# Kernel tuning notes

Measured on AMD Instinct MI355X. Metric: run time of the kernel, lower is better.

## Reference

```python
import jax, jax.numpy as jnp
import numpy as np

jax.config.update("jax_enable_x64", True)  # original computes distances in float64

B, NL, NP, C, H, G, A, E = 16, 64, 512, 128, 256, 10, 14, 2048
BN_EPS = 1e-5


def _static_indices():
    # ragged graph sizes (batch_num_nodes) -> static scatter / valid-pair indices
    counts_l = np.array([32 if i % 2 == 0 else 64 for i in range(B)])
    counts_p = np.array([256 if i % 2 == 0 else 512 for i in range(B)])
    idx_l = np.concatenate([b * NL + np.arange(c) for b, c in enumerate(counts_l)])
    idx_p = np.concatenate([b * NP + np.arange(c) for b, c in enumerate(counts_p)])
    mask_l = np.zeros(B * NL, bool); mask_l[idx_l] = True
    mask_p = np.zeros(B * NP, bool); mask_p[idx_p] = True
    mask = mask_l.reshape(B, NL, 1) & mask_p.reshape(B, 1, NP)  # C_mask
    pair_flat = np.nonzero(mask.reshape(-1))[0]                 # row-major == torch C[C_mask] order
    pb = pair_flat // (NL * NP)
    rem = pair_flat % (NL * NP)
    pair_l = pb * NL + rem // NP
    pair_p = pb * NP + rem % NP
    return idx_l, idx_p, pair_flat, pair_l, pair_p, pb, len(idx_l), len(idx_p)


def setup_inputs() -> dict:
    idx_l, idx_p, pair_flat, pair_l, pair_p, pair_b, TL, TP = _static_indices()
    ks = jax.random.split(jax.random.key(0), 14)
    f32 = jnp.float32
    s = 0.02
    return {
        "h_l": jax.random.normal(ks[0], (TL, C), f32),
        "h_p": jax.random.normal(ks[1], (TP, C), f32),
        "lig_pos": jax.random.normal(ks[2], (TL, 3), f32) * 5.0,
        "prot_pos": jax.random.normal(ks[3], (TP, A, 3), f32) * 5.0,
        "edge_src": jax.random.randint(ks[4], (E,), 0, TL),
        "edge_dst": jax.random.randint(ks[5], (E,), 0, TL),
        "idx_l": jnp.asarray(idx_l), "idx_p": jnp.asarray(idx_p),
        "pair_flat": jnp.asarray(pair_flat), "pair_l": jnp.asarray(pair_l),
        "pair_p": jnp.asarray(pair_p), "pair_b": jnp.asarray(pair_b),
        "W1": jax.random.normal(ks[6], (2 * C, H), f32) * s, "b1": jnp.zeros(H, f32),
        "gamma": jnp.ones(H, f32), "beta": jnp.zeros(H, f32),
        "rmean": jnp.zeros(H, f32), "rvar": jnp.ones(H, f32),
        "Wpi": jax.random.normal(ks[7], (H, G * A), f32) * s, "bpi": jnp.zeros(G * A, f32),
        "Wsig": jax.random.normal(ks[8], (H, G * A), f32) * s, "bsig": jnp.zeros(G * A, f32),
        "Wmu": jax.random.normal(ks[9], (H, G * A), f32) * s, "bmu": jnp.zeros(G * A, f32),
        "Wat": jax.random.normal(ks[10], (C, 17), f32) * s, "bat": jnp.zeros(17, f32),
        "Wbt": jax.random.normal(ks[11], (2 * C, 5), f32) * s, "bbt": jnp.zeros(5, f32),
    }


def reference(h_l, h_p, lig_pos, prot_pos, edge_src, edge_dst, idx_l, idx_p,
              pair_flat, pair_l, pair_p, pair_b, W1, b1, gamma, beta, rmean, rvar,
              Wpi, bpi, Wsig, bsig, Wmu, bmu, Wat, bat, Wbt, bbt):
    # scatter ragged node feats into padded dense batches (to_dense_batch_dgl)
    dense_l = jnp.zeros((B * NL, C), h_l.dtype).at[idx_l].set(h_l)
    dense_p = jnp.zeros((B * NP, C), h_p.dtype).at[idx_p].set(h_p)
    # gather only valid (ligand, protein) pairs instead of the dense [B,NL,NP,2C] tensor
    Cpair = jnp.concatenate([dense_l[pair_l], dense_p[pair_p]], axis=-1)  # [M, 2C]
    x = Cpair @ W1 + b1
    x = gamma * (x - rmean) / jnp.sqrt(rvar + BN_EPS) + beta  # BatchNorm1d (eval)
    x = jax.nn.elu(x)                                          # dropout off (eval)
    pi = jax.nn.softmax(x @ Wpi + bpi, axis=-1).reshape(-1, G, A)
    sigma = (jax.nn.elu(x @ Wsig + bsig) + 1.1).reshape(-1, G, A)
    mu = (jax.nn.elu(x @ Wmu + bmu) + 1.0).reshape(-1, G, A)
    atom_types = h_l @ Wat + bat                               # [TL, 17]
    bond_types = jnp.concatenate([h_l[edge_src], h_l[edge_dst]], -1) @ Wbt + bbt  # [E, 5]
    # euclidean distance matrix in float64, as in the original
    X = jnp.zeros((B * NL, 3), jnp.float64).at[idx_l].set(lig_pos.astype(jnp.float64)).reshape(B, NL, 3)
    Y = jnp.zeros((B * NP, A, 3), jnp.float64).at[idx_p].set(prot_pos.astype(jnp.float64)).reshape(B, NP * A, 3)
    d2 = (-2.0 * jnp.einsum('bld,bpd->blp', X, Y)
          + jnp.sum(Y * Y, -1)[:, None, :] + jnp.sum(X * X, -1)[:, :, None])
    dist = jnp.nan_to_num(jnp.sqrt(d2), nan=10000.0).reshape(B * NL * NP, A)[pair_flat]
    dist = jax.lax.stop_gradient(dist[:, None, :])             # [M, 1, A], detached
    return (pi, sigma, mu, dist, atom_types, bond_types, pair_b)
```

## Files before the change

kernel.cpp:

```cpp
#include <hip/hip_runtime.h>


typedef __attribute__((ext_vector_type(4))) float f32x4;
typedef __attribute__((ext_vector_type(4))) unsigned int u32x4;
typedef __attribute__((ext_vector_type(8))) short bf16x8;

#define M_TOT 327680
#define WSCALE 16.0f
#define WDESCALE 0.0625f

__device__ __forceinline__ unsigned short f2bf(float f) {
    union { float f; unsigned int u; } v; v.f = f;
    unsigned int r = (v.u + 0x7FFFu + ((v.u >> 16) & 1u)) >> 16;
    return (unsigned short)r;
}

__device__ __forceinline__ float eluf(float y) {
    return fmaxf(y, 0.f) + __expf(fminf(y, 0.f)) - 1.f;
}

__device__ __forceinline__ float bfhalf_lo(unsigned int u) {
    return __uint_as_float(u << 16);
}
__device__ __forceinline__ float bfhalf_hi(unsigned int u) {
    return __uint_as_float(u & 0xFFFF0000u);
}

__global__ void prep_weights(const float* __restrict__ W1, const float* __restrict__ b1,
                             const float* __restrict__ gamma, const float* __restrict__ beta,
                             const float* __restrict__ rmean, const float* __restrict__ rvar,
                             const float* __restrict__ Wpi, const float* __restrict__ bpi,
                             const float* __restrict__ Wsig, const float* __restrict__ bsig,
                             const float* __restrict__ Wmu, const float* __restrict__ bmu,
                             const float* __restrict__ h_l,
                             const int* __restrict__ esrc, const int* __restrict__ edst,
                             const float* __restrict__ Wat, const float* __restrict__ bat,
                             const float* __restrict__ Wbt, const float* __restrict__ bbt,
                             unsigned short* __restrict__ W1T, unsigned char* __restrict__ W2q,
                             float* __restrict__ b2s, float* __restrict__ a1v, float* __restrict__ csv,
                             float* __restrict__ out_at, float* __restrict__ out_bt) {
    int idx = blockIdx.x * 256 + threadIdx.x;
    {
        int j    = idx & 7;
        int h    = (idx >> 3) & 1;
        int lane = (idx >> 4) & 63;
        int sp   = (idx >> 10) & 3;
        int t    = idx >> 12;
        int f    = t % 9;
        int head = t / 9;
        int k    = (sp * 2 + h) * 32 + (lane >> 4) * 8 + j;
        int col  = f * 16 + (lane & 15);
        float v = 0.f;
        if (col < 140) {
            const float* Wh = (head == 0) ? Wpi : (head == 1) ? Wsig : Wmu;
            v = Wh[k * 140 + col] * WSCALE;
        }
        W2q[idx] = (unsigned char)(__builtin_amdgcn_cvt_pk_fp8_f32(v, 0.f, 0, false) & 0xFF);
    }
    if (idx < 256 * 256) {
        int n = idx >> 8, k = idx & 255;
        W1T[idx] = f2bf(W1[k * 256 + n]);
    }
    if (idx < 432) {
        int head = idx / 144, col = idx % 144;
        float v = 0.f;
        if (col < 140) v = (head == 0) ? bpi[col] : (head == 1) ? bsig[col] : bmu[col];
        b2s[idx] = v * WSCALE;
    }
    if (idx < 256) {
        float s = gamma[idx] * rsqrtf(rvar[idx] + 1e-5f);
        a1v[idx] = s;
        csv[idx] = s * (b1[idx] - rmean[idx]) + beta[idx];
    }
    if (idx < 768 * 17) {
        int row = idx / 17, c = idx % 17;
        const float* hr = h_l + (size_t)row * 128;
        float s = bat[c];
        #pragma unroll 4
        for (int k = 0; k < 128; ++k) s += hr[k] * Wat[k * 17 + c];
        out_at[idx] = s;
    } else if (idx < 768 * 17 + 2048 * 5) {
        int t2 = idx - 768 * 17;
        int e = t2 / 5, c = t2 % 5;
        const float* hs = h_l + (size_t)esrc[e] * 128;
        const float* hd = h_l + (size_t)edst[e] * 128;
        float s = bbt[c];
        #pragma unroll 4
        for (int k = 0; k < 128; ++k)
            s += hs[k] * Wbt[k * 5 + c] + hd[k] * Wbt[(k + 128) * 5 + c];
        out_bt[t2] = s;
    }
}

__global__ __launch_bounds__(256, 2) void node_gemm(
        const float* __restrict__ h_l, const float* __restrict__ h_p,
        const unsigned short* __restrict__ W1T,
        const float* __restrict__ a1v, const float* __restrict__ csv,
        unsigned short* __restrict__ Lq, unsigned short* __restrict__ Pq) {
    const int tid = threadIdx.x, lane = tid & 63, w = tid >> 6;
    const int cGrp = lane & 15, g = lane >> 4;
    const int row0 = blockIdx.x * 64;
    const bool isLig = row0 < 768;
    const float* src = isLig ? (h_l + (size_t)row0 * 128) : (h_p + (size_t)(row0 - 768) * 128);
    unsigned short* dst = isLig ? (Lq + (size_t)row0 * 256) : (Pq + (size_t)(row0 - 768) * 256);
    const int koff = isLig ? 0 : 128;

    f32x4 acc[16];
    #pragma unroll
    for (int fn = 0; fn < 16; ++fn) acc[fn] = (f32x4){0.f, 0.f, 0.f, 0.f};

    #pragma unroll
    for (int fk = 0; fk < 4; ++fk) {
        const float* ap = src + (size_t)(w * 16 + cGrp) * 128 + fk * 32 + g * 8;
        f32x4 qa = *(const f32x4*)ap;
        f32x4 qb = *(const f32x4*)(ap + 4);
        bf16x8 af;
        af[0] = (short)f2bf(qa[0]); af[1] = (short)f2bf(qa[1]);
        af[2] = (short)f2bf(qa[2]); af[3] = (short)f2bf(qa[3]);
        af[4] = (short)f2bf(qb[0]); af[5] = (short)f2bf(qb[1]);
        af[6] = (short)f2bf(qb[2]); af[7] = (short)f2bf(qb[3]);
        #pragma unroll
        for (int fn = 0; fn < 16; ++fn) {
            bf16x8 bf = *(const bf16x8*)(W1T + (fn * 16 + cGrp) * 256 + koff + fk * 32 + g * 8);
            acc[fn] = __builtin_amdgcn_mfma_f32_16x16x32_bf16(af, bf, acc[fn], 0, 0, 0);
        }
    }
    #pragma unroll
    for (int fn = 0; fn < 16; ++fn) {
        int h = fn * 16 + cGrp;
        float s = a1v[h];
        float c0 = isLig ? csv[h] : 0.f;
        #pragma unroll
        for (int rg = 0; rg < 4; ++rg)
            dst[(size_t)(w * 16 + g * 4 + rg) * 256 + h] = f2bf(s * acc[fn][rg] + c0);
    }
}

__global__ __launch_bounds__(256, 4) void pair_kernel(
        const unsigned short* __restrict__ Lq, const unsigned short* __restrict__ Pq,
        const unsigned char* __restrict__ W2q, const float* __restrict__ b2s,
        const float* __restrict__ lig_pos, const float* __restrict__ prot_pos,
        float* __restrict__ out_pi, float* __restrict__ out_sig, float* __restrict__ out_mu,
        float* __restrict__ out_dist, float* __restrict__ out_pb) {

    __shared__ __align__(16) unsigned char Bs[36864];

    const int tid = threadIdx.x, lane = tid & 63, w = tid >> 6;
    const int c = lane & 15, g = lane >> 4;
    const int head = blockIdx.y;
    const int m0 = blockIdx.x * 64;

    unsigned int P = (unsigned int)m0 / 40960u;
    unsigned int r = (unsigned int)m0 % 40960u;
    int b, cl, cp0;
    if (r < 8192u) {
        b = 2 * (int)P; cl = 96 * (int)P + (int)(r >> 8); cp0 = 768 * (int)P + (int)(r & 255u);
    } else {
        unsigned int rr = r - 8192u;
        b = 2 * (int)P + 1; cl = 96 * (int)P + 32 + (int)(rr >> 9);
        cp0 = 768 * (int)P + 256 + (int)(rr & 511u);
    }

    const unsigned char* wsrc = W2q + (size_t)head * 36864;
    u32x4 stg[9];
    #pragma unroll
    for (int i = 0; i < 9; ++i)
        stg[i] = *(const u32x4*)(wsrc + (size_t)(tid + 256 * i) * 16);

    float bb[9];
    #pragma unroll
    for (int f = 0; f < 9; ++f) bb[f] = b2s[head * 144 + f * 16 + c];

    const int row = w * 16 + c;
    const unsigned short* pqp = Pq + (size_t)(cp0 + row) * 256;
    const unsigned short* lqp = Lq + (size_t)cl * 256;
    long Xa[8];
    #pragma unroll
    for (int s = 0; s < 8; ++s) {
        u32x4 pv = *(const u32x4*)(pqp + s * 32 + g * 8);
        u32x4 lv = *(const u32x4*)(lqp + s * 32 + g * 8);
        float y0 = eluf(bfhalf_lo(pv[0]) + bfhalf_lo(lv[0]));
        float y1 = eluf(bfhalf_hi(pv[0]) + bfhalf_hi(lv[0]));
        float y2 = eluf(bfhalf_lo(pv[1]) + bfhalf_lo(lv[1]));
        float y3 = eluf(bfhalf_hi(pv[1]) + bfhalf_hi(lv[1]));
        float y4 = eluf(bfhalf_lo(pv[2]) + bfhalf_lo(lv[2]));
        float y5 = eluf(bfhalf_hi(pv[2]) + bfhalf_hi(lv[2]));
        float y6 = eluf(bfhalf_lo(pv[3]) + bfhalf_lo(lv[3]));
        float y7 = eluf(bfhalf_hi(pv[3]) + bfhalf_hi(lv[3]));
        unsigned int lo = (unsigned int)__builtin_amdgcn_cvt_pk_fp8_f32(y0, y1, 0, false);
        lo = (unsigned int)__builtin_amdgcn_cvt_pk_fp8_f32(y2, y3, (int)lo, true);
        unsigned int hi = (unsigned int)__builtin_amdgcn_cvt_pk_fp8_f32(y4, y5, 0, false);
        hi = (unsigned int)__builtin_amdgcn_cvt_pk_fp8_f32(y6, y7, (int)hi, true);
        Xa[s] = (long)(((unsigned long long)hi << 32) | (unsigned long long)lo);
    }

    #pragma unroll
    for (int i = 0; i < 9; ++i)
        *(u32x4*)(Bs + (size_t)(tid + 256 * i) * 16) = stg[i];
    __syncthreads();

    f32x4 acc[9];
    #pragma unroll
    for (int f = 0; f < 9; ++f) acc[f] = (f32x4){bb[f], bb[f], bb[f], bb[f]};

    #pragma unroll
    for (int sp = 0; sp < 4; ++sp) {
        long xa0 = Xa[2 * sp], xa1 = Xa[2 * sp + 1];
        #pragma unroll
        for (int f = 0; f < 9; ++f) {
            u32x4 bq = *(const u32x4*)(Bs + f * 4096 + sp * 1024 + lane * 16);
            long b0 = (long)(((unsigned long long)bq[1] << 32) | (unsigned long long)bq[0]);
            long b1 = (long)(((unsigned long long)bq[3] << 32) | (unsigned long long)bq[2]);
            acc[f] = __builtin_amdgcn_mfma_f32_16x16x32_fp8_fp8(xa0, b0, acc[f], 0, 0, 0);
            acc[f] = __builtin_amdgcn_mfma_f32_16x16x32_fp8_fp8(xa1, b1, acc[f], 0, 0, 0);
        }
    }

    #pragma unroll
    for (int f = 0; f < 9; ++f)
        #pragma unroll
        for (int q = 0; q < 4; ++q) acc[f][q] *= WDESCALE;

    const bool v8 = (c < 12);

    if (head == 0) {
        #pragma unroll
        for (int q = 0; q < 4; ++q) {
            float mx = fmaxf(fmaxf(fmaxf(acc[0][q], acc[1][q]), fmaxf(acc[2][q], acc[3][q])),
                             fmaxf(fmaxf(acc[4][q], acc[5][q]), fmaxf(acc[6][q], acc[7][q])));
            if (v8) mx = fmaxf(mx, acc[8][q]);
            mx = fmaxf(mx, __shfl_xor(mx, 1, 64));
            mx = fmaxf(mx, __shfl_xor(mx, 2, 64));
            mx = fmaxf(mx, __shfl_xor(mx, 4, 64));
            mx = fmaxf(mx, __shfl_xor(mx, 8, 64));
            float e0 = __expf(acc[0][q] - mx), e1 = __expf(acc[1][q] - mx);
            float e2 = __expf(acc[2][q] - mx), e3 = __expf(acc[3][q] - mx);
            float e4 = __expf(acc[4][q] - mx), e5 = __expf(acc[5][q] - mx);
            float e6 = __expf(acc[6][q] - mx), e7 = __expf(acc[7][q] - mx);
            float e8 = v8 ? __expf(acc[8][q] - mx) : 0.f;
            float sm = ((e0 + e1) + (e2 + e3)) + ((e4 + e5) + (e6 + e7)) + e8;
            sm += __shfl_xor(sm, 1, 64);
            sm += __shfl_xor(sm, 2, 64);
            sm += __shfl_xor(sm, 4, 64);
            sm += __shfl_xor(sm, 8, 64);
            float inv = 1.f / sm;
            const int gr = m0 + w * 16 + g * 4 + q;
            float* prow = out_pi + (size_t)gr * 140;
            prow[c]       = e0 * inv;  prow[16 + c]  = e1 * inv;
            prow[32 + c]  = e2 * inv;  prow[48 + c]  = e3 * inv;
            prow[64 + c]  = e4 * inv;  prow[80 + c]  = e5 * inv;
            prow[96 + c]  = e6 * inv;  prow[112 + c] = e7 * inv;
            if (v8) prow[128 + c] = e8 * inv;
        }
    } else if (head == 1) {
        #pragma unroll
        for (int q = 0; q < 4; ++q) {
            const int gr = m0 + w * 16 + g * 4 + q;
            float* srow = out_sig + (size_t)gr * 140;
            srow[c]       = eluf(acc[0][q]) + 1.1f;
            srow[16 + c]  = eluf(acc[1][q]) + 1.1f;
            srow[32 + c]  = eluf(acc[2][q]) + 1.1f;
            srow[48 + c]  = eluf(acc[3][q]) + 1.1f;
            srow[64 + c]  = eluf(acc[4][q]) + 1.1f;
            srow[80 + c]  = eluf(acc[5][q]) + 1.1f;
            srow[96 + c]  = eluf(acc[6][q]) + 1.1f;
            srow[112 + c] = eluf(acc[7][q]) + 1.1f;
            if (v8) srow[128 + c] = eluf(acc[8][q]) + 1.1f;
        }
    } else {
        #pragma unroll
        for (int q = 0; q < 4; ++q) {
            const int gr = m0 + w * 16 + g * 4 + q;
            float* mrow = out_mu + (size_t)gr * 140;
            mrow[c]       = eluf(acc[0][q]) + 1.0f;
            mrow[16 + c]  = eluf(acc[1][q]) + 1.0f;
            mrow[32 + c]  = eluf(acc[2][q]) + 1.0f;
            mrow[48 + c]  = eluf(acc[3][q]) + 1.0f;
            mrow[64 + c]  = eluf(acc[4][q]) + 1.0f;
            mrow[80 + c]  = eluf(acc[5][q]) + 1.0f;
            mrow[96 + c]  = eluf(acc[6][q]) + 1.0f;
            mrow[112 + c] = eluf(acc[7][q]) + 1.0f;
            if (v8) mrow[128 + c] = eluf(acc[8][q]) + 1.0f;
        }
        float lx = lig_pos[cl * 3 + 0];
        float ly = lig_pos[cl * 3 + 1];
        float lz = lig_pos[cl * 3 + 2];
        for (int idx = tid; idx < 64 * 14; idx += 256) {
            int rw = idx / 14, a = idx - rw * 14;
            const float* pp = prot_pos + (size_t)(cp0 + rw) * 42 + a * 3;
            float dx = lx - pp[0], dy = ly - pp[1], dz = lz - pp[2];
            out_dist[(size_t)(m0 + rw) * 14 + a] = sqrtf(dx * dx + dy * dy + dz * dz);
        }
        if (tid < 64) out_pb[m0 + tid] = (float)b;
    }
}

extern "C" void kernel_launch(void* const* d_in, const int* in_sizes, int n_in,
                              void* d_out, int out_size, void* d_ws, size_t ws_size,
                              hipStream_t stream) {
    const float* h_l      = (const float*)d_in[0];
    const float* h_p      = (const float*)d_in[1];
    const float* lig_pos  = (const float*)d_in[2];
    const float* prot_pos = (const float*)d_in[3];
    const int*   esrc     = (const int*)d_in[4];
    const int*   edst     = (const int*)d_in[5];
    const float* W1    = (const float*)d_in[12];
    const float* b1    = (const float*)d_in[13];
    const float* gamma = (const float*)d_in[14];
    const float* beta  = (const float*)d_in[15];
    const float* rmean = (const float*)d_in[16];
    const float* rvar  = (const float*)d_in[17];
    const float* Wpi   = (const float*)d_in[18];
    const float* bpi   = (const float*)d_in[19];
    const float* Wsig  = (const float*)d_in[20];
    const float* bsig  = (const float*)d_in[21];
    const float* Wmu   = (const float*)d_in[22];
    const float* bmu   = (const float*)d_in[23];
    const float* Wat   = (const float*)d_in[24];
    const float* bat   = (const float*)d_in[25];
    const float* Wbt   = (const float*)d_in[26];
    const float* bbt   = (const float*)d_in[27];

    char* ws = (char*)d_ws;
    unsigned short* W1T = (unsigned short*)(ws + 0);
    unsigned char*  W2q = (unsigned char*)(ws + 131072);
    float*          b2s = (float*)(ws + 241664);
    float*          a1v = (float*)(ws + 243392);
    float*          csv = (float*)(ws + 244416);
    unsigned short* Lq  = (unsigned short*)(ws + 245440);
    unsigned short* Pq  = (unsigned short*)(ws + 638656);

    float* out = (float*)d_out;
    const size_t M = M_TOT;
    float* out_pi   = out;
    float* out_sig  = out + M * 140;
    float* out_mu   = out + 2 * M * 140;
    float* out_dist = out + 3 * M * 140;
    float* out_at   = out + 3 * M * 140 + M * 14;
    float* out_bt   = out_at + 768 * 17;
    float* out_pb   = out_bt + 2048 * 5;

    hipLaunchKernelGGL(prep_weights, dim3(432), dim3(256), 0, stream,
                       W1, b1, gamma, beta, rmean, rvar,
                       Wpi, bpi, Wsig, bsig, Wmu, bmu,
                       h_l, esrc, edst, Wat, bat, Wbt, bbt,
                       W1T, W2q, b2s, a1v, csv, out_at, out_bt);

    hipLaunchKernelGGL(node_gemm, dim3((768 + 6144) / 64), dim3(256), 0, stream,
                       h_l, h_p, W1T, a1v, csv, Lq, Pq);

    hipLaunchKernelGGL(pair_kernel, dim3(M_TOT / 64, 3), dim3(256), 0, stream,
                       Lq, Pq, W2q, b2s, lig_pos, prot_pos,
                       out_pi, out_sig, out_mu, out_dist, out_pb);
}
```

Baseline: 207.1 us.

## Precompute fp8 pair activations once and share across head kernels

Splits the pair stage into a kernel that builds the fp8 ELU pair activations, distances and batch ids once per row block, and a second kernel that runs the per-head fp8 MFMA GEMM reading those activations from workspace. This removes the threefold recomputation of the gather/ELU/quantize work across heads. In exchange it writes and re-reads a large intermediate buffer through memory and adds a launch; it falls back to the fused kernel if the workspace is too small.

Measured after the change: 260.2 us. 25.7% more time.

```diff
diff --git a/kernel.cpp b/kernel.cpp
--- a/kernel.cpp
+++ b/kernel.cpp
@@ -4,6 +4,7 @@
 typedef __attribute__((ext_vector_type(4))) float f32x4;
 typedef __attribute__((ext_vector_type(4))) unsigned int u32x4;
 typedef __attribute__((ext_vector_type(8))) short bf16x8;
+typedef __attribute__((ext_vector_type(2))) long i64x2;
 
 #define M_TOT 327680
 #define WSCALE 16.0f
@@ -136,23 +137,9 @@
     }
 }
 
-__global__ __launch_bounds__(256, 4) void pair_kernel(
-        const unsigned short* __restrict__ Lq, const unsigned short* __restrict__ Pq,
-        const unsigned char* __restrict__ W2q, const float* __restrict__ b2s,
-        const float* __restrict__ lig_pos, const float* __restrict__ prot_pos,
-        float* __restrict__ out_pi, float* __restrict__ out_sig, float* __restrict__ out_mu,
-        float* __restrict__ out_dist, float* __restrict__ out_pb) {
-
-    __shared__ __align__(16) unsigned char Bs[36864];
-
-    const int tid = threadIdx.x, lane = tid & 63, w = tid >> 6;
-    const int c = lane & 15, g = lane >> 4;
-    const int head = blockIdx.y;
-    const int m0 = blockIdx.x * 64;
-
+__device__ __forceinline__ void pair_decode(int m0, int& b, int& cl, int& cp0) {
     unsigned int P = (unsigned int)m0 / 40960u;
     unsigned int r = (unsigned int)m0 % 40960u;
-    int b, cl, cp0;
     if (r < 8192u) {
         b = 2 * (int)P; cl = 96 * (int)P + (int)(r >> 8); cp0 = 768 * (int)P + (int)(r & 255u);
     } else {
@@ -160,20 +147,24 @@
         b = 2 * (int)P + 1; cl = 96 * (int)P + 32 + (int)(rr >> 9);
         cp0 = 768 * (int)P + 256 + (int)(rr & 511u);
     }
-
-    const unsigned char* wsrc = W2q + (size_t)head * 36864;
-    u32x4 stg[9];
-    #pragma unroll
-    for (int i = 0; i < 9; ++i)
-        stg[i] = *(const u32x4*)(wsrc + (size_t)(tid + 256 * i) * 16);
-
-    float bb[9];
-    #pragma unroll
-    for (int f = 0; f < 9; ++f) bb[f] = b2s[head * 144 + f * 16 + c];
+}
+
+__global__ __launch_bounds__(256, 4) void xq_kernel(
+        const unsigned short* __restrict__ Lq, const unsigned short* __restrict__ Pq,
+        const float* __restrict__ lig_pos, const float* __restrict__ prot_pos,
+        unsigned char* __restrict__ Xq,
+        float* __restrict__ out_dist, float* __restrict__ out_pb) {
+    const int tid = threadIdx.x, lane = tid & 63, w = tid >> 6;
+    const int c = lane & 15, g = lane >> 4;
+    const int m0 = blockIdx.x * 64;
+
+    int b, cl, cp0;
+    pair_decode(m0, b, cl, cp0);
 
     const int row = w * 16 + c;
     const unsigned short* pqp = Pq + (size_t)(cp0 + row) * 256;
     const unsigned short* lqp = Lq + (size_t)cl * 256;
+
     long Xa[8];
     #pragma unroll
     for (int s = 0; s < 8; ++s) {
@@ -194,6 +185,52 @@
         Xa[s] = (long)(((unsigned long long)hi << 32) | (unsigned long long)lo);
     }
 
+    unsigned char* xp = Xq + (size_t)blockIdx.x * 16384 + tid * 16;
+    #pragma unroll
+    for (int j = 0; j < 4; ++j) {
+        i64x2 q; q[0] = Xa[2 * j]; q[1] = Xa[2 * j + 1];
+        *(i64x2*)(xp + j * 4096) = q;
+    }
+
+    float lx = lig_pos[cl * 3 + 0];
+    float ly = lig_pos[cl * 3 + 1];
+    float lz = lig_pos[cl * 3 + 2];
+    for (int idx = tid; idx < 64 * 14; idx += 256) {
+        int rw = idx / 14, a = idx - rw * 14;
+        const float* pp = prot_pos + (size_t)(cp0 + rw) * 42 + a * 3;
+        float dx = lx - pp[0], dy = ly - pp[1], dz = lz - pp[2];
+        out_dist[(size_t)(m0 + rw) * 14 + a] = sqrtf(dx * dx + dy * dy + dz * dz);
+    }
+    if (tid < 64) out_pb[m0 + tid] = (float)b;
+}
+
+__global__ __launch_bounds__(256, 4) void pair_kernel_xq(
+        const unsigned char* __restrict__ Xq,
+        const unsigned char* __restrict__ W2q, const float* __restrict__ b2s,
+        float* __restrict__ out_pi, float* __restrict__ out_sig, float* __restrict__ out_mu) {
+
+    __shared__ __align__(16) unsigned char Bs[36864];
+
+    const int tid = threadIdx.x, lane = tid & 63, w = tid >> 6;
+    const int c = lane & 15, g = lane >> 4;
+    const int head = blockIdx.y;
+    const int m0 = blockIdx.x * 64;
+
+    const unsigned char* xp = Xq + (size_t)blockIdx.x * 16384 + tid * 16;
+    i64x2 xa[4];
+    #pragma unroll
+    for (int j = 0; j < 4; ++j) xa[j] = *(const i64x2*)(xp + j * 4096);
+
+    const unsigned char* wsrc = W2q + (size_t)head * 36864;
+    u32x4 stg[9];
+    #pragma unroll
+    for (int i = 0; i < 9; ++i)
+        stg[i] = *(const u32x4*)(wsrc + (size_t)(tid + 256 * i) * 16);
+
+    float bb[9];
+    #pragma unroll
+    for (int f = 0; f < 9; ++f) bb[f] = b2s[head * 144 + f * 16 + c];
+
     #pragma unroll
     for (int i = 0; i < 9; ++i)
         *(u32x4*)(Bs + (size_t)(tid + 256 * i) * 16) = stg[i];
@@ -205,7 +242,7 @@
 
     #pragma unroll
     for (int sp = 0; sp < 4; ++sp) {
-        long xa0 = Xa[2 * sp], xa1 = Xa[2 * sp + 1];
+        long xa0 = xa[sp][0], xa1 = xa[sp][1];
         #pragma unroll
         for (int f = 0; f < 9; ++f) {
             u32x4 bq = *(const u32x4*)(Bs + f * 4096 + sp * 1024 + lane * 16);
@@ -252,6 +289,134 @@
             prow[96 + c]  = e6 * inv;  prow[112 + c] = e7 * inv;
             if (v8) prow[128 + c] = e8 * inv;
         }
+    } else {
+        float addc = (head == 1) ? 1.1f : 1.0f;
+        float* outh = (head == 1) ? out_sig : out_mu;
+        #pragma unroll
+        for (int q = 0; q < 4; ++q) {
+            const int gr = m0 + w * 16 + g * 4 + q;
+            float* row = outh + (size_t)gr * 140;
+            row[c]       = eluf(acc[0][q]) + addc;
+            row[16 + c]  = eluf(acc[1][q]) + addc;
+            row[32 + c]  = eluf(acc[2][q]) + addc;
+            row[48 + c]  = eluf(acc[3][q]) + addc;
+            row[64 + c]  = eluf(acc[4][q]) + addc;
+            row[80 + c]  = eluf(acc[5][q]) + addc;
+            row[96 + c]  = eluf(acc[6][q]) + addc;
+            row[112 + c] = eluf(acc[7][q]) + addc;
+            if (v8) row[128 + c] = eluf(acc[8][q]) + addc;
+        }
+    }
+}
+
+__global__ __launch_bounds__(256, 4) void pair_kernel_fused(
+        const unsigned short* __restrict__ Lq, const unsigned short* __restrict__ Pq,
+        const unsigned char* __restrict__ W2q, const float* __restrict__ b2s,
+        const float* __restrict__ lig_pos, const float* __restrict__ prot_pos,
+        float* __restrict__ out_pi, float* __restrict__ out_sig, float* __restrict__ out_mu,
+        float* __restrict__ out_dist, float* __restrict__ out_pb) {
+
+    __shared__ __align__(16) unsigned char Bs[36864];
+
+    const int tid = threadIdx.x, lane = tid & 63, w = tid >> 6;
+    const int c = lane & 15, g = lane >> 4;
+    const int head = blockIdx.y;
+    const int m0 = blockIdx.x * 64;
+
+    int b, cl, cp0;
+    pair_decode(m0, b, cl, cp0);
+
+    const unsigned char* wsrc = W2q + (size_t)head * 36864;
+    u32x4 stg[9];
+    #pragma unroll
+    for (int i = 0; i < 9; ++i)
+        stg[i] = *(const u32x4*)(wsrc + (size_t)(tid + 256 * i) * 16);
+
+    float bb[9];
+    #pragma unroll
+    for (int f = 0; f < 9; ++f) bb[f] = b2s[head * 144 + f * 16 + c];
+
+    const int row = w * 16 + c;
+    const unsigned short* pqp = Pq + (size_t)(cp0 + row) * 256;
+    const unsigned short* lqp = Lq + (size_t)cl * 256;
+    long Xa[8];
+    #pragma unroll
+    for (int s = 0; s < 8; ++s) {
+        u32x4 pv = *(const u32x4*)(pqp + s * 32 + g * 8);
+        u32x4 lv = *(const u32x4*)(lqp + s * 32 + g * 8);
+        float y0 = eluf(bfhalf_lo(pv[0]) + bfhalf_lo(lv[0]));
+        float y1 = eluf(bfhalf_hi(pv[0]) + bfhalf_hi(lv[0]));
+        float y2 = eluf(bfhalf_lo(pv[1]) + bfhalf_lo(lv[1]));
+        float y3 = eluf(bfhalf_hi(pv[1]) + bfhalf_hi(lv[1]));
+        float y4 = eluf(bfhalf_lo(pv[2]) + bfhalf_lo(lv[2]));
+        float y5 = eluf(bfhalf_hi(pv[2]) + bfhalf_hi(lv[2]));
+        float y6 = eluf(bfhalf_lo(pv[3]) + bfhalf_lo(lv[3]));
+        float y7 = eluf(bfhalf_hi(pv[3]) + bfhalf_hi(lv[3]));
+        unsigned int lo = (unsigned int)__builtin_amdgcn_cvt_pk_fp8_f32(y0, y1, 0, false);
+        lo = (unsigned int)__builtin_amdgcn_cvt_pk_fp8_f32(y2, y3, (int)lo, true);
+        unsigned int hi = (unsigned int)__builtin_amdgcn_cvt_pk_fp8_f32(y4, y5, 0, false);
+        hi = (unsigned int)__builtin_amdgcn_cvt_pk_fp8_f32(y6, y7, (int)hi, true);
+        Xa[s] = (long)(((unsigned long long)hi << 32) | (unsigned long long)lo);
+    }
+
+    #pragma unroll
+    for (int i = 0; i < 9; ++i)
+        *(u32x4*)(Bs + (size_t)(tid + 256 * i) * 16) = stg[i];
+    __syncthreads();
+
+    f32x4 acc[9];
+    #pragma unroll
+    for (int f = 0; f < 9; ++f) acc[f] = (f32x4){bb[f], bb[f], bb[f], bb[f]};
+
+    #pragma unroll
+    for (int sp = 0; sp < 4; ++sp) {
+        long xa0 = Xa[2 * sp], xa1 = Xa[2 * sp + 1];
+        #pragma unroll
+        for (int f = 0; f < 9; ++f) {
+            u32x4 bq = *(const u32x4*)(Bs + f * 4096 + sp * 1024 + lane * 16);
+            long b0 = (long)(((unsigned long long)bq[1] << 32) | (unsigned long long)bq[0]);
+            long b1 = (long)(((unsigned long long)bq[3] << 32) | (unsigned long long)bq[2]);
+            acc[f] = __builtin_amdgcn_mfma_f32_16x16x32_fp8_fp8(xa0, b0, acc[f], 0, 0, 0);
+            acc[f] = __builtin_amdgcn_mfma_f32_16x16x32_fp8_fp8(xa1, b1, acc[f], 0, 0, 0);
+        }
+    }
+
+    #pragma unroll
+    for (int f = 0; f < 9; ++f)
+        #pragma unroll
+        for (int q = 0; q < 4; ++q) acc[f][q] *= WDESCALE;
+
+    const bool v8 = (c < 12);
+
+    if (head == 0) {
+        #pragma unroll
+        for (int q = 0; q < 4; ++q) {
+            float mx = fmaxf(fmaxf(fmaxf(acc[0][q], acc[1][q]), fmaxf(acc[2][q], acc[3][q])),
+                             fmaxf(fmaxf(acc[4][q], acc[5][q]), fmaxf(acc[6][q], acc[7][q])));
+            if (v8) mx = fmaxf(mx, acc[8][q]);
+            mx = fmaxf(mx, __shfl_xor(mx, 1, 64));
+            mx = fmaxf(mx, __shfl_xor(mx, 2, 64));
+            mx = fmaxf(mx, __shfl_xor(mx, 4, 64));
+            mx = fmaxf(mx, __shfl_xor(mx, 8, 64));
+            float e0 = __expf(acc[0][q] - mx), e1 = __expf(acc[1][q] - mx);
+            float e2 = __expf(acc[2][q] - mx), e3 = __expf(acc[3][q] - mx);
+            float e4 = __expf(acc[4][q] - mx), e5 = __expf(acc[5][q] - mx);
+            float e6 = __expf(acc[6][q] - mx), e7 = __expf(acc[7][q] - mx);
+            float e8 = v8 ? __expf(acc[8][q] - mx) : 0.f;
+            float sm = ((e0 + e1) + (e2 + e3)) + ((e4 + e5) + (e6 + e7)) + e8;
+            sm += __shfl_xor(sm, 1, 64);
+            sm += __shfl_xor(sm, 2, 64);
+            sm += __shfl_xor(sm, 4, 64);
+            sm += __shfl_xor(sm, 8, 64);
+            float inv = 1.f / sm;
+            const int gr = m0 + w * 16 + g * 4 + q;
+            float* prow = out_pi + (size_t)gr * 140;
+            prow[c]       = e0 * inv;  prow[16 + c]  = e1 * inv;
+            prow[32 + c]  = e2 * inv;  prow[48 + c]  = e3 * inv;
+            prow[64 + c]  = e4 * inv;  prow[80 + c]  = e5 * inv;
+            prow[96 + c]  = e6 * inv;  prow[112 + c] = e7 * inv;
+            if (v8) prow[128 + c] = e8 * inv;
+        }
     } else if (head == 1) {
         #pragma unroll
         for (int q = 0; q < 4; ++q) {
@@ -329,6 +494,8 @@
     float*          csv = (float*)(ws + 244416);
     unsigned short* Lq  = (unsigned short*)(ws + 245440);
     unsigned short* Pq  = (unsigned short*)(ws + 638656);
+    unsigned char*  Xq  = (unsigned char*)(ws + 3784448);
+    const size_t WS_NEED = 3784448ULL + 83886080ULL;
 
     float* out = (float*)d_out;
     const size_t M = M_TOT;
@@ -349,7 +516,14 @@
     hipLaunchKernelGGL(node_gemm, dim3((768 + 6144) / 64), dim3(256), 0, stream,
                        h_l, h_p, W1T, a1v, csv, Lq, Pq);
 
-    hipLaunchKernelGGL(pair_kernel, dim3(M_TOT / 64, 3), dim3(256), 0, stream,
-                       Lq, Pq, W2q, b2s, lig_pos, prot_pos,
-                       out_pi, out_sig, out_mu, out_dist, out_pb);
-}
+    if (ws_size >= WS_NEED) {
+        hipLaunchKernelGGL(xq_kernel, dim3(M_TOT / 64), dim3(256), 0, stream,
+                           Lq, Pq, lig_pos, prot_pos, Xq, out_dist, out_pb);
+        hipLaunchKernelGGL(pair_kernel_xq, dim3(M_TOT / 64, 3), dim3(256), 0, stream,
+                           Xq, W2q, b2s, out_pi, out_sig, out_mu);
+    } else {
+        hipLaunchKernelGGL(pair_kernel_fused, dim3(M_TOT / 64, 3), dim3(256), 0, stream,
+                           Lq, Pq, W2q, b2s, lig_pos, prot_pos,
+                           out_pi, out_sig, out_mu, out_dist, out_pb);
+    }
+}
```

## Split distance computation into separate kernel and interleave pair-kernel heads

Applied to the files above, without the earlier changes.

Moves the distance and batch-index output out of the mu-head blocks of the pair kernel into a dedicated dist_kernel, so the three heads do equal work. The pair grid is flattened so that the three heads for the same 64-row tile are adjacent in launch order, which may improve L2 reuse of Lq/Pq. node_gemm is split in half along the output dimension to double its block count. W1T transposition now reads W1 coalesced and writes scattered. Together these rebalance load and add one more kernel launch.

After: 211.7 us. 1.02x slower.

```diff
diff --git a/kernel.cpp b/kernel.cpp
--- a/kernel.cpp
+++ b/kernel.cpp
@@ -24,6 +24,18 @@
 }
 __device__ __forceinline__ float bfhalf_hi(unsigned int u) {
     return __uint_as_float(u & 0xFFFF0000u);
+}
+
+__device__ __forceinline__ void pair_decode(int m0, int& b, int& cl, int& cp0) {
+    unsigned int P = (unsigned int)m0 / 40960u;
+    unsigned int r = (unsigned int)m0 % 40960u;
+    if (r < 8192u) {
+        b = 2 * (int)P; cl = 96 * (int)P + (int)(r >> 8); cp0 = 768 * (int)P + (int)(r & 255u);
+    } else {
+        unsigned int rr = r - 8192u;
+        b = 2 * (int)P + 1; cl = 96 * (int)P + 32 + (int)(rr >> 9);
+        cp0 = 768 * (int)P + 256 + (int)(rr & 511u);
+    }
 }
 
 __global__ void prep_weights(const float* __restrict__ W1, const float* __restrict__ b1,
@@ -58,8 +70,8 @@
         W2q[idx] = (unsigned char)(__builtin_amdgcn_cvt_pk_fp8_f32(v, 0.f, 0, false) & 0xFF);
     }
     if (idx < 256 * 256) {
-        int n = idx >> 8, k = idx & 255;
-        W1T[idx] = f2bf(W1[k * 256 + n]);
+        int n = idx & 255, k = idx >> 8;
+        W1T[n * 256 + k] = f2bf(W1[k * 256 + n]);
     }
     if (idx < 432) {
         int head = idx / 144, col = idx % 144;
@@ -99,15 +111,16 @@
         unsigned short* __restrict__ Lq, unsigned short* __restrict__ Pq) {
     const int tid = threadIdx.x, lane = tid & 63, w = tid >> 6;
     const int cGrp = lane & 15, g = lane >> 4;
-    const int row0 = blockIdx.x * 64;
+    const int nh   = blockIdx.x & 1;
+    const int row0 = (blockIdx.x >> 1) * 64;
     const bool isLig = row0 < 768;
     const float* src = isLig ? (h_l + (size_t)row0 * 128) : (h_p + (size_t)(row0 - 768) * 128);
     unsigned short* dst = isLig ? (Lq + (size_t)row0 * 256) : (Pq + (size_t)(row0 - 768) * 256);
     const int koff = isLig ? 0 : 128;
 
-    f32x4 acc[16];
-    #pragma unroll
-    for (int fn = 0; fn < 16; ++fn) acc[fn] = (f32x4){0.f, 0.f, 0.f, 0.f};
+    f32x4 acc[8];
+    #pragma unroll
+    for (int fn = 0; fn < 8; ++fn) acc[fn] = (f32x4){0.f, 0.f, 0.f, 0.f};
 
     #pragma unroll
     for (int fk = 0; fk < 4; ++fk) {
@@ -120,46 +133,61 @@
         af[4] = (short)f2bf(qb[0]); af[5] = (short)f2bf(qb[1]);
         af[6] = (short)f2bf(qb[2]); af[7] = (short)f2bf(qb[3]);
         #pragma unroll
-        for (int fn = 0; fn < 16; ++fn) {
-            bf16x8 bf = *(const bf16x8*)(W1T + (fn * 16 + cGrp) * 256 + koff + fk * 32 + g * 8);
+        for (int fn = 0; fn < 8; ++fn) {
+            int n = nh * 128 + fn * 16 + cGrp;
+            bf16x8 bf = *(const bf16x8*)(W1T + (size_t)n * 256 + koff + fk * 32 + g * 8);
             acc[fn] = __builtin_amdgcn_mfma_f32_16x16x32_bf16(af, bf, acc[fn], 0, 0, 0);
         }
     }
     #pragma unroll
-    for (int fn = 0; fn < 16; ++fn) {
-        int h = fn * 16 + cGrp;
+    for (int fn = 0; fn < 8; ++fn) {
+        int h = nh * 128 + fn * 16 + cGrp;
         float s = a1v[h];
         float c0 = isLig ? csv[h] : 0.f;
         #pragma unroll
         for (int rg = 0; rg < 4; ++rg)
             dst[(size_t)(w * 16 + g * 4 + rg) * 256 + h] = f2bf(s * acc[fn][rg] + c0);
     }
+}
+
+__global__ __launch_bounds__(256, 8) void dist_kernel(
+        const float* __restrict__ lig_pos, const float* __restrict__ prot_pos,
+        float* __restrict__ out_dist, float* __restrict__ out_pb) {
+    const int m0 = blockIdx.x * 256;
+    int b, cl, cp0;
+    pair_decode(m0, b, cl, cp0);
+
+    const int rw = threadIdx.x;
+    float lx = lig_pos[cl * 3 + 0];
+    float ly = lig_pos[cl * 3 + 1];
+    float lz = lig_pos[cl * 3 + 2];
+    const float* pp = prot_pos + (size_t)(cp0 + rw) * 42;
+    float* dr = out_dist + (size_t)(m0 + rw) * 14;
+    #pragma unroll
+    for (int a = 0; a < 14; ++a) {
+        float dx = lx - pp[a * 3 + 0];
+        float dy = ly - pp[a * 3 + 1];
+        float dz = lz - pp[a * 3 + 2];
+        dr[a] = sqrtf(dx * dx + dy * dy + dz * dz);
+    }
+    out_pb[m0 + rw] = (float)b;
 }
 
 __global__ __launch_bounds__(256, 4) void pair_kernel(
         const unsigned short* __restrict__ Lq, const unsigned short* __restrict__ Pq,
         const unsigned char* __restrict__ W2q, const float* __restrict__ b2s,
-        const float* __restrict__ lig_pos, const float* __restrict__ prot_pos,
-        float* __restrict__ out_pi, float* __restrict__ out_sig, float* __restrict__ out_mu,
-        float* __restrict__ out_dist, float* __restrict__ out_pb) {
+        float* __restrict__ out_pi, float* __restrict__ out_sig, float* __restrict__ out_mu) {
 
     __shared__ __align__(16) unsigned char Bs[36864];
 
     const int tid = threadIdx.x, lane = tid & 63, w = tid >> 6;
     const int c = lane & 15, g = lane >> 4;
-    const int head = blockIdx.y;
-    const int m0 = blockIdx.x * 64;
-
-    unsigned int P = (unsigned int)m0 / 40960u;
-    unsigned int r = (unsigned int)m0 % 40960u;
+    const unsigned int bid = blockIdx.x;
+    const int head = (int)(bid % 3u);
+    const int m0   = (int)(bid / 3u) * 64;
+
     int b, cl, cp0;
-    if (r < 8192u) {
-        b = 2 * (int)P; cl = 96 * (int)P + (int)(r >> 8); cp0 = 768 * (int)P + (int)(r & 255u);
-    } else {
-        unsigned int rr = r - 8192u;
-        b = 2 * (int)P + 1; cl = 96 * (int)P + 32 + (int)(rr >> 9);
-        cp0 = 768 * (int)P + 256 + (int)(rr & 511u);
-    }
+    pair_decode(m0, b, cl, cp0);
 
     const unsigned char* wsrc = W2q + (size_t)head * 36864;
     u32x4 stg[9];
@@ -252,46 +280,23 @@
             prow[96 + c]  = e6 * inv;  prow[112 + c] = e7 * inv;
             if (v8) prow[128 + c] = e8 * inv;
         }
-    } else if (head == 1) {
+    } else {
+        const float addc = (head == 1) ? 1.1f : 1.0f;
+        float* outh = (head == 1) ? out_sig : out_mu;
         #pragma unroll
         for (int q = 0; q < 4; ++q) {
             const int gr = m0 + w * 16 + g * 4 + q;
-            float* srow = out_sig + (size_t)gr * 140;
-            srow[c]       = eluf(acc[0][q]) + 1.1f;
-            srow[16 + c]  = eluf(acc[1][q]) + 1.1f;
-            srow[32 + c]  = eluf(acc[2][q]) + 1.1f;
-            srow[48 + c]  = eluf(acc[3][q]) + 1.1f;
-            srow[64 + c]  = eluf(acc[4][q]) + 1.1f;
-            srow[80 + c]  = eluf(acc[5][q]) + 1.1f;
-            srow[96 + c]  = eluf(acc[6][q]) + 1.1f;
-            srow[112 + c] = eluf(acc[7][q]) + 1.1f;
-            if (v8) srow[128 + c] = eluf(acc[8][q]) + 1.1f;
-        }
-    } else {
-        #pragma unroll
-        for (int q = 0; q < 4; ++q) {
-            const int gr = m0 + w * 16 + g * 4 + q;
-            float* mrow = out_mu + (size_t)gr * 140;
-            mrow[c]       = eluf(acc[0][q]) + 1.0f;
-            mrow[16 + c]  = eluf(acc[1][q]) + 1.0f;
-            mrow[32 + c]  = eluf(acc[2][q]) + 1.0f;
-            mrow[48 + c]  = eluf(acc[3][q]) + 1.0f;
-            mrow[64 + c]  = eluf(acc[4][q]) + 1.0f;
-            mrow[80 + c]  = eluf(acc[5][q]) + 1.0f;
-            mrow[96 + c]  = eluf(acc[6][q]) + 1.0f;
-            mrow[112 + c] = eluf(acc[7][q]) + 1.0f;
-            if (v8) mrow[128 + c] = eluf(acc[8][q]) + 1.0f;
-        }
-        float lx = lig_pos[cl * 3 + 0];
-        float ly = lig_pos[cl * 3 + 1];
-        float lz = lig_pos[cl * 3 + 2];
-        for (int idx = tid; idx < 64 * 14; idx += 256) {
-            int rw = idx / 14, a = idx - rw * 14;
-            const float* pp = prot_pos + (size_t)(cp0 + rw) * 42 + a * 3;
-            float dx = lx - pp[0], dy = ly - pp[1], dz = lz - pp[2];
-            out_dist[(size_t)(m0 + rw) * 14 + a] = sqrtf(dx * dx + dy * dy + dz * dz);
-        }
-        if (tid < 64) out_pb[m0 + tid] = (float)b;
+            float* row = outh + (size_t)gr * 140;
+            row[c]       = eluf(acc[0][q]) + addc;
+            row[16 + c]  = eluf(acc[1][q]) + addc;
+            row[32 + c]  = eluf(acc[2][q]) + addc;
+            row[48 + c]  = eluf(acc[3][q]) + addc;
+            row[64 + c]  = eluf(acc[4][q]) + addc;
+            row[80 + c]  = eluf(acc[5][q]) + addc;
+            row[96 + c]  = eluf(acc[6][q]) + addc;
+            row[112 + c] = eluf(acc[7][q]) + addc;
+            if (v8) row[128 + c] = eluf(acc[8][q]) + addc;
+        }
     }
 }
 
@@ -340,16 +345,18 @@
     float* out_bt   = out_at + 768 * 17;
     float* out_pb   = out_bt + 2048 * 5;
 
+    hipLaunchKernelGGL(dist_kernel, dim3(M_TOT / 256), dim3(256), 0, stream,
+                       lig_pos, prot_pos, out_dist, out_pb);
+
     hipLaunchKernelGGL(prep_weights, dim3(432), dim3(256), 0, stream,
                        W1, b1, gamma, beta, rmean, rvar,
                        Wpi, bpi, Wsig, bsig, Wmu, bmu,
                        h_l, esrc, edst, Wat, bat, Wbt, bbt,
                        W1T, W2q, b2s, a1v, csv, out_at, out_bt);
 
-    hipLaunchKernelGGL(node_gemm, dim3((768 + 6144) / 64), dim3(256), 0, stream,
+    hipLaunchKernelGGL(node_gemm, dim3(2 * (768 + 6144) / 64), dim3(256), 0, stream,
                        h_l, h_p, W1T, a1v, csv, Lq, Pq);
 
-    hipLaunchKernelGGL(pair_kernel, dim3(M_TOT / 64, 3), dim3(256), 0, stream,
-                       Lq, Pq, W2q, b2s, lig_pos, prot_pos,
-                       out_pi, out_sig, out_mu, out_dist, out_pb);
-}
+    hipLaunchKernelGGL(pair_kernel, dim3(3 * M_TOT / 64), dim3(256), 0, stream,
+                       Lq, Pq, W2q, b2s, out_pi, out_sig, out_mu);
+}
```
